# Kernel optimization log

Measured on AMD Instinct MI355X. Metric: run time of the kernel, lower is better.

The kernel has to match this reference:

```python
import jax, jax.numpy as jnp
import numpy as np

B, T, IN_DIM = 8, 1024, 512
NUM_HEADS, H_DIM = 8, 64
OUT_DIM = NUM_HEADS * H_DIM
MAX_POS = 512


def setup_inputs() -> dict:
    key = jax.random.key(0)
    ks = jax.random.split(key, 9)
    s = 0.02
    return {
        "x": jax.random.normal(ks[0], (B, T, IN_DIM), dtype=jnp.float32),
        "Wq": jax.random.normal(ks[1], (IN_DIM, OUT_DIM), dtype=jnp.float32) * s,
        "bq": jax.random.normal(ks[2], (OUT_DIM,), dtype=jnp.float32) * s,
        "Wkv": jax.random.normal(ks[3], (IN_DIM, 2 * OUT_DIM), dtype=jnp.float32) * s,
        "bkv": jax.random.normal(ks[4], (2 * OUT_DIM,), dtype=jnp.float32) * s,
        "Wout": jax.random.normal(ks[5], (OUT_DIM, IN_DIM), dtype=jnp.float32) * s,
        "bout": jax.random.normal(ks[6], (IN_DIM,), dtype=jnp.float32) * s,
        "rel_emb": jax.random.normal(ks[7], (2 * MAX_POS + 1, H_DIM), dtype=jnp.float32) * s,
    }


def reference(x, Wq, bq, Wkv, bkv, Wout, bout, rel_emb):
    b, t, _ = x.shape
    scale = H_DIM ** -0.5
    q = x @ Wq + bq                      # [b, t, H*D]
    kv = x @ Wkv + bkv                   # [b, t, 2*H*D]
    k, v = jnp.split(kv, 2, axis=-1)

    def split_heads(a):
        return a.reshape(b, t, NUM_HEADS, H_DIM).transpose(0, 2, 1, 3)  # b h t d

    q, k, v = map(split_heads, (q, k, v))
    dots = jnp.einsum("bhnd,bhmd->bhnm", q, k) * scale

    seq = jnp.arange(t)
    dist = jnp.clip(seq[:, None] - seq[None, :], -MAX_POS, MAX_POS) + MAX_POS  # [n, m]
    rel_pos = rel_emb[dist]              # [n, m, d]
    pos_attn = jnp.einsum("bhnd,nmd->bhnm", q, rel_pos) * scale

    attn = jax.nn.softmax(dots + pos_attn, axis=-1)
    out = jnp.einsum("bhnm,bhmd->bhnd", attn, v)
    out = out.transpose(0, 2, 1, 3).reshape(b, t, OUT_DIM)
    return out @ Wout + bout             # dropout p=0 -> identity
```

## Files before the change

kernel.cpp:

```cpp
#include <hip/hip_runtime.h>

#define BB 8
#define TT 1024
#define NH 8
#define HD 64
#define QT 128

typedef unsigned short u16;
typedef __attribute__((ext_vector_type(8))) short bf16x8;
typedef __attribute__((ext_vector_type(16))) float f32x16;

__device__ __forceinline__ float bf2f(u16 s) {
    union { unsigned u; float f; } v; v.u = ((unsigned)s) << 16; return v.f;
}
__device__ __forceinline__ u16 f2bf(float f) {
    union { float f; unsigned u; } v; v.f = f;
    unsigned r = (v.u + 0x7FFFu + ((v.u >> 16) & 1u)) >> 16;
    return (u16)r;
}
__device__ __forceinline__ float bperm(int byte_idx, float v) {
    union { float f; int i; } a; a.f = v;
    union { int i; float f; } b;
    b.i = __builtin_amdgcn_ds_bpermute(byte_idx, a.i);
    return b.f;
}
__device__ __forceinline__ void gload_lds16(const u16* g, u16* l) {
    __builtin_amdgcn_global_load_lds(
        (const __attribute__((address_space(1))) unsigned int*)g,
        (__attribute__((address_space(3))) unsigned int*)l, 16, 0, 0);
}

#define MFMA(a, b, c) __builtin_amdgcn_mfma_f32_32x32x16_bf16((a), (b), (c), 0, 0, 0)

#define NX4 1048576
#define NR4 16400
__global__ void cvt_misc(const float* __restrict__ x, const float* __restrict__ rel,
                         u16* __restrict__ xb, u16* __restrict__ relb)
{
    size_t i = (size_t)blockIdx.x * 256 + threadIdx.x;
    const float* src; u16* dst;
    if (i < NX4) { src = x; dst = xb; }
    else {
        i -= NX4;
        if (i >= NR4) return;
        src = rel; dst = relb;
    }
    float4 f = *(const float4*)(src + i * 4);
    ushort4 o;
    o.x = f2bf(f.x); o.y = f2bf(f.y); o.z = f2bf(f.z); o.w = f2bf(f.w);
    *(ushort4*)(dst + i * 4) = o;
}

__global__ __launch_bounds__(256) void cvt_wT(
    const float* __restrict__ Wq, const float* __restrict__ Wkv,
    const float* __restrict__ Wout,
    u16* __restrict__ WqT, u16* __restrict__ WkvT, u16* __restrict__ WoutT)
{
    __shared__ float tile[64][65];
    int bid = blockIdx.x;
    const float* W; u16* Wt; int N, kt, ct;
    if (bid < 64)       { W = Wq;   Wt = WqT;   N = 512;  kt = (bid >> 3) * 64; ct = (bid & 7) * 64; }
    else if (bid < 192) { bid -= 64;  W = Wkv;  Wt = WkvT; N = 1024; kt = (bid >> 4) * 64; ct = (bid & 15) * 64; }
    else                { bid -= 192; W = Wout; Wt = WoutT; N = 512;  kt = (bid >> 3) * 64; ct = (bid & 7) * 64; }

    const int tid = threadIdx.x;
#pragma unroll
    for (int i = 0; i < 16; i++) {
        int e = tid + i * 256;
        int r = e >> 6, c = e & 63;
        tile[r][c] = W[(size_t)(kt + r) * N + ct + c];
    }
    __syncthreads();
#pragma unroll
    for (int i = 0; i < 16; i++) {
        int e = tid + i * 256;
        int rr = e >> 6, cc = e & 63;
        Wt[(size_t)(ct + rr) * 512 + kt + cc] = f2bf(tile[cc][rr]);
    }
}

#define GEMM_STAGE(As, Bs, Abase, Bbase, k0)                                   \
    {                                                                          \
        const int wb16 = (tid & 192) * 8;   \
        _Pragma("unroll")                                                      \
        for (int i = 0; i < 4; i++) {                                          \
            int slot = i * 256 + tid;                                          \
            int row = slot >> 3;                                               \
            int c16 = (slot & 7) ^ (row & 7);                                  \
            gload_lds16(Abase + (size_t)row * 512 + (k0) + c16 * 8,            \
                        As + i * 2048 + wb16);                                 \
            gload_lds16(Bbase + (size_t)row * 512 + (k0) + c16 * 8,            \
                        Bs + i * 2048 + wb16);                                 \
        }                                                                      \
    }

#define GEMM_COMPUTE(As, Bs, ar_base, br_base)                                 \
    {                                                                          \
        _Pragma("unroll")                                                      \
        for (int ks = 0; ks < 4; ks++) {                                       \
            bf16x8 a0, a1, b0, b1;                                             \
            {                                                                  \
                int r0_ = (ar_base), r1_ = (ar_base) + 32;                     \
                int q0_ = (br_base), q1_ = (br_base) + 32;                     \
                a0 = *(const bf16x8*)(As + r0_ * 64 +                          \
                                      (((2 * ks + lh) ^ (r0_ & 7)) * 8));      \
                a1 = *(const bf16x8*)(As + r1_ * 64 +                          \
                                      (((2 * ks + lh) ^ (r1_ & 7)) * 8));      \
                b0 = *(const bf16x8*)(Bs + q0_ * 64 +                          \
                                      (((2 * ks + lh) ^ (q0_ & 7)) * 8));      \
                b1 = *(const bf16x8*)(Bs + q1_ * 64 +                          \
                                      (((2 * ks + lh) ^ (q1_ & 7)) * 8));      \
            }                                                                  \
            acc[0][0] = MFMA(a0, b0, acc[0][0]);                               \
            acc[0][1] = MFMA(a0, b1, acc[0][1]);                               \
            acc[1][0] = MFMA(a1, b0, acc[1][0]);                               \
            acc[1][1] = MFMA(a1, b1, acc[1][1]);                               \
        }                                                                      \
    }

__global__ __launch_bounds__(256) void gemm_qkv(
    const u16* __restrict__ A, const u16* __restrict__ Bt,
    const float* __restrict__ bq, const float* __restrict__ bkv,
    u16* __restrict__ oq, u16* __restrict__ ok, u16* __restrict__ ov)
{
    __shared__ __align__(16) u16 As[128 * 64];
    __shared__ __align__(16) u16 Bs[128 * 64];

    const int tid = threadIdx.x;
    const int lane = tid & 63, w = tid >> 6;
    const int l31 = lane & 31, lh = lane >> 5;
    const int wr = w & 1, wc = w >> 1;
    const int row0 = blockIdx.x * 128 + 64 * wr;
    const int c0g  = blockIdx.y * 128 + 64 * wc;

    const u16* Abase = A  + (size_t)blockIdx.x * 128 * 512;
    const u16* Bbase = Bt + (size_t)blockIdx.y * 128 * 512;
    const int ar_base = 64 * wr + l31;
    const int br_base = 64 * wc + l31;

    f32x16 acc[2][2];
#pragma unroll
    for (int i = 0; i < 2; i++)
#pragma unroll
        for (int j = 0; j < 2; j++)
#pragma unroll
            for (int e = 0; e < 16; e++) acc[i][j][e] = 0.f;

    for (int kk = 0; kk < 8; kk++) {
        GEMM_STAGE(As, Bs, Abase, Bbase, kk * 64);
        __syncthreads();
        GEMM_COMPUTE(As, Bs, ar_base, br_base);
        __syncthreads();
    }

    const int rbase = 4 * lh;
#pragma unroll
    for (int ri = 0; ri < 2; ri++) {
#pragma unroll
        for (int ci = 0; ci < 2; ci++) {
            const int r0 = row0 + 32 * ri;
            const int gc = c0g + 32 * ci + l31;
            if (gc < 512) {
                const float bv = bq[gc];
                const int h = gc >> 6, d = gc & 63;
#pragma unroll
                for (int rg = 0; rg < 16; rg++) {
                    int gr = r0 + (rg & 3) + 8 * (rg >> 2) + rbase;
                    int b = gr >> 10, t = gr & 1023;
                    oq[(((size_t)b * NH + h) * TT + t) * HD + d] =
                        f2bf((acc[ri][ci][rg] + bv) * 0.18033688f);
                }
            } else if (gc < 1024) {
                const float bv = bkv[gc - 512];
                const int h = (gc - 512) >> 6, d = gc & 63;
#pragma unroll
                for (int rg = 0; rg < 16; rg++) {
                    int gr = r0 + (rg & 3) + 8 * (rg >> 2) + rbase;
                    int b = gr >> 10, t = gr & 1023;
                    ok[(((size_t)b * NH + h) * TT + t) * HD + d] =
                        f2bf(acc[ri][ci][rg] + bv);
                }
            } else {
                const float bv = bkv[gc - 512];
                const int vcol = gc - 1024;
                const int h = vcol >> 6, d = vcol & 63;
                const int b = r0 >> 10;
                const int t0 = (r0 & 1023) + rbase;
                size_t base = (((size_t)b * NH + h) * HD + d) * TT;
#pragma unroll
                for (int g = 0; g < 4; g++) {
                    ushort4 p;
                    p.x = f2bf(acc[ri][ci][4 * g + 0] + bv);
                    p.y = f2bf(acc[ri][ci][4 * g + 1] + bv);
                    p.z = f2bf(acc[ri][ci][4 * g + 2] + bv);
                    p.w = f2bf(acc[ri][ci][4 * g + 3] + bv);
                    *(ushort4*)&ov[base + t0 + 8 * g] = p;
                }
            }
        }
    }
}

__global__ __launch_bounds__(256) void gemm_out(
    const u16* __restrict__ A, const u16* __restrict__ Bt,
    const float* __restrict__ bias, float* __restrict__ of)
{
    __shared__ __align__(16) u16 As[128 * 64];
    __shared__ __align__(16) u16 Bs[128 * 64];

    const int tid = threadIdx.x;
    const int lane = tid & 63, w = tid >> 6;
    const int l31 = lane & 31, lh = lane >> 5;
    const int wr = w & 1, wc = w >> 1;
    const int row0 = blockIdx.x * 128 + 64 * wr;
    const int c0g  = blockIdx.y * 128 + 64 * wc;

    const u16* Abase = A  + (size_t)blockIdx.x * 128 * 512;
    const u16* Bbase = Bt + (size_t)blockIdx.y * 128 * 512;
    const int ar_base = 64 * wr + l31;
    const int br_base = 64 * wc + l31;

    f32x16 acc[2][2];
#pragma unroll
    for (int i = 0; i < 2; i++)
#pragma unroll
        for (int j = 0; j < 2; j++)
#pragma unroll
            for (int e = 0; e < 16; e++) acc[i][j][e] = 0.f;

    for (int kk = 0; kk < 8; kk++) {
        GEMM_STAGE(As, Bs, Abase, Bbase, kk * 64);
        __syncthreads();
        GEMM_COMPUTE(As, Bs, ar_base, br_base);
        __syncthreads();
    }

    const int rbase = 4 * lh;
#pragma unroll
    for (int ri = 0; ri < 2; ri++) {
#pragma unroll
        for (int ci = 0; ci < 2; ci++) {
            const int gcol = c0g + 32 * ci + l31;
            const float bv = bias[gcol];
#pragma unroll
            for (int rg = 0; rg < 16; rg++) {
                int gr = row0 + 32 * ri + (rg & 3) + 8 * (rg >> 2) + rbase;
                of[(size_t)gr * 512 + gcol] = acc[ri][ci][rg] + bv;
            }
        }
    }
}

__global__ __launch_bounds__(256) void attn_mfma(
    const u16* __restrict__ q_ws, const u16* __restrict__ k_ws,
    const u16* __restrict__ v_ws, const u16* __restrict__ relb,
    u16* __restrict__ attn_out)
{
    __shared__ __align__(16) u16 GPs[4][32 * 104];

    const int tid  = threadIdx.x;
    const int lane = tid & 63;
    const int w    = tid >> 6;
    const int l31  = lane & 31;
    const int lh   = lane >> 5;
    const int bh   = blockIdx.x;
    const int n0   = blockIdx.y * QT;

    const unsigned lin = blockIdx.y * 64 + blockIdx.x;
    const int off = (int)((lin * 2654435761u) >> 24) & 15;

    bf16x8 a_q[4];
    {
        const u16* qp = q_ws + (((size_t)bh * TT) + n0 + 32 * w + l31) * HD + 8 * lh;
#pragma unroll
        for (int ks = 0; ks < 4; ks++)
            a_q[ks] = *(const bf16x8*)(qp + 16 * ks);
    }

    f32x16 O0, O1;
    float li[16];
#pragma unroll
    for (int i = 0; i < 16; i++) { O0[i] = 0.f; O1[i] = 0.f; li[i] = 0.f; }

    u16* Gw = GPs[w];
    const int rbase = 4 * lh;
    const u16* kbase = k_ws + (size_t)bh * TT * HD;
    const u16* vbase = v_ws + (size_t)bh * HD * TT;
    const int pbb = n0 + 449 + 32 * w;

    f32x16 zvec;
#pragma unroll
    for (int i = 0; i < 16; i++) zvec[i] = 0.f;
    int bidx16[16];
#pragma unroll
    for (int rg = 0; rg < 16; rg++) {
        int r = (rg & 3) + 8 * (rg >> 2) + rbase;
        bidx16[rg] = (((lh << 5) | ((r - l31 + 31) & 31))) << 2;
    }

    bf16x8 kf[8], rf[12];
    {
        const u16* kb = kbase + (size_t)(off * 64) * HD;
#pragma unroll
        for (int ks = 0; ks < 4; ks++) {
            const int doff = 16 * ks + 8 * lh;
            kf[2 * ks]     = *(const bf16x8*)(kb + (size_t)l31 * HD + doff);
            kf[2 * ks + 1] = *(const bf16x8*)(kb + (size_t)(l31 + 32) * HD + doff);
        }
    }
    f32x16 S0 = MFMA(a_q[0], kf[0], zvec);
    f32x16 S1 = MFMA(a_q[0], kf[1], zvec);
#pragma unroll
    for (int ks = 1; ks < 4; ks++) {
        S0 = MFMA(a_q[ks], kf[2 * ks], S0);
        S1 = MFMA(a_q[ks], kf[2 * ks + 1], S1);
    }
    {
        const int pb = pbb - off * 64;
#pragma unroll
        for (int gt = 0; gt < 3; gt++) {
            int p = pb + 32 * gt + l31;
            p = p < 0 ? 0 : (p > 1024 ? 1024 : p);
            const u16* rb = relb + (size_t)p * HD;
#pragma unroll
            for (int ks = 0; ks < 4; ks++)
                rf[4 * gt + ks] = *(const bf16x8*)(rb + 16 * ks + 8 * lh);
        }
    }
    {
        const u16* kb = kbase + (size_t)(((off + 1) & 15) * 64) * HD;
#pragma unroll
        for (int ks = 0; ks < 4; ks++) {
            const int doff = 16 * ks + 8 * lh;
            kf[2 * ks]     = *(const bf16x8*)(kb + (size_t)l31 * HD + doff);
            kf[2 * ks + 1] = *(const bf16x8*)(kb + (size_t)(l31 + 32) * HD + doff);
        }
    }

    for (int it = 0; it < 16; it++) {
        const int mt = (off + it) & 15;
        const int m0 = mt * 64;

        f32x16 gA = MFMA(a_q[0], rf[0], zvec);
        f32x16 gB = MFMA(a_q[0], rf[4], zvec);
        f32x16 gC = MFMA(a_q[0], rf[8], zvec);
#pragma unroll
        for (int ks = 1; ks < 4; ks++) {
            gA = MFMA(a_q[ks], rf[ks], gA);
            gB = MFMA(a_q[ks], rf[4 + ks], gB);
            gC = MFMA(a_q[ks], rf[8 + ks], gC);
        }

#pragma unroll
        for (int rg = 0; rg < 16; rg++) {
            int r = (rg & 3) + 8 * (rg >> 2) + rbase;
            float mS0 = (l31 >= r) ? gB[rg] : gC[rg];
            float mS1 = (l31 >= r) ? gA[rg] : gB[rg];
            S0[rg] += bperm(bidx16[rg], mS0);
            S1[rg] += bperm(bidx16[rg], mS1);
        }

        bf16x8 vf[8];
        {
            const u16* vb = vbase + m0;
#pragma unroll
            for (int ms = 0; ms < 4; ms++) {
                const int mg = 2 * ms + lh;
                vf[2 * ms]     = *(const bf16x8*)(vb + (size_t)l31 * TT + mg * 8);
                vf[2 * ms + 1] = *(const bf16x8*)(vb + (size_t)(l31 + 32) * TT + mg * 8);
            }
        }
        {
            const int m0n = ((off + it + 1) & 15) * 64;
            const int pb = pbb - m0n;
#pragma unroll
            for (int gt = 0; gt < 3; gt++) {
                int p = pb + 32 * gt + l31;
                p = p < 0 ? 0 : (p > 1024 ? 1024 : p);
                const u16* rb = relb + (size_t)p * HD;
#pragma unroll
                for (int ks = 0; ks < 4; ks++)
                    rf[4 * gt + ks] = *(const bf16x8*)(rb + 16 * ks + 8 * lh);
            }
        }

#pragma unroll
        for (int rg = 0; rg < 16; rg++) {
            float e0, e1;
            asm("v_exp_f32 %0, %1" : "=v"(e0) : "v"(S0[rg]));
            asm("v_exp_f32 %0, %1" : "=v"(e1) : "v"(S1[rg]));
            li[rg] += e0 + e1;
            unsigned pk;
            asm("v_cvt_pk_bf16_f32 %0, %1, %2" : "=v"(pk) : "v"(e0), "v"(e1));
            int r = (rg & 3) + 8 * (rg >> 2) + rbase;
            Gw[r * 104 + (((l31 >> 3) ^ (r & 7)) * 8) + (l31 & 7)] = (u16)pk;
            Gw[r * 104 + (((((l31 + 32) >> 3)) ^ (r & 7)) * 8) + (l31 & 7)] =
                (u16)(pk >> 16);
        }

        if (it < 15) {
            __builtin_amdgcn_s_setprio(1);
            S0 = MFMA(a_q[0], kf[0], zvec);
            S1 = MFMA(a_q[0], kf[1], zvec);
#pragma unroll
            for (int ks = 1; ks < 4; ks++) {
                S0 = MFMA(a_q[ks], kf[2 * ks], S0);
                S1 = MFMA(a_q[ks], kf[2 * ks + 1], S1);
            }
            __builtin_amdgcn_s_setprio(0);
            const int m0k = ((off + it + 2) & 15) * 64;
            const u16* kb = kbase + (size_t)m0k * HD;
#pragma unroll
            for (int ks = 0; ks < 4; ks++) {
                const int doff = 16 * ks + 8 * lh;
                kf[2 * ks]     = *(const bf16x8*)(kb + (size_t)l31 * HD + doff);
                kf[2 * ks + 1] = *(const bf16x8*)(kb + (size_t)(l31 + 32) * HD + doff);
            }
        }

        __builtin_amdgcn_s_setprio(1);
#pragma unroll
        for (int ms = 0; ms < 4; ms++) {
            const int mg = 2 * ms + lh;
            bf16x8 a_p = *(const bf16x8*)&Gw[l31 * 104 + ((mg ^ (l31 & 7)) * 8)];
            O0 = MFMA(a_p, vf[2 * ms], O0);
            O1 = MFMA(a_p, vf[2 * ms + 1], O1);
        }
        __builtin_amdgcn_s_setprio(0);
    }

#pragma unroll
    for (int rg = 0; rg < 16; rg++) {
        float rs = li[rg];
        rs += __shfl_xor(rs, 1);
        rs += __shfl_xor(rs, 2);
        rs += __shfl_xor(rs, 4);
        rs += __shfl_xor(rs, 8);
        rs += __shfl_xor(rs, 16);
        li[rg] = 1.0f / rs;
    }

    const int b = bh >> 3, h = bh & 7;
    u16* ob = attn_out + ((size_t)b * TT + n0 + 32 * w) * 512 + h * 64;
#pragma unroll
    for (int rg = 0; rg < 16; rg++) {
        int r = (rg & 3) + 8 * (rg >> 2) + rbase;
        ob[(size_t)r * 512 + l31]      = f2bf(O0[rg] * li[rg]);
        ob[(size_t)r * 512 + l31 + 32] = f2bf(O1[rg] * li[rg]);
    }
}

extern "C" void kernel_launch(void* const* d_in, const int* in_sizes, int n_in,
                              void* d_out, int out_size, void* d_ws, size_t ws_size,
                              hipStream_t stream)
{
    const float* x    = (const float*)d_in[0];
    const float* Wq   = (const float*)d_in[1];
    const float* bq   = (const float*)d_in[2];
    const float* Wkv  = (const float*)d_in[3];
    const float* bkv  = (const float*)d_in[4];
    const float* Wout = (const float*)d_in[5];
    const float* bout = (const float*)d_in[6];
    const float* rel  = (const float*)d_in[7];
    float* out = (float*)d_out;

    char* ws = (char*)d_ws;
    const size_t MB = 1024 * 1024;
    u16*   q_wsb  = (u16*)(ws);
    u16*   k_wsb  = (u16*)(ws + 8 * MB);
    u16*   v_wsb  = (u16*)(ws + 16 * MB);
    u16*   x_bf   = (u16*)(ws + 24 * MB);
    u16*   a_wsb  = (u16*)(ws + 32 * MB);
    u16*   relb   = (u16*)(ws + 40 * MB);
    u16*   WT_all = (u16*)(ws + 41 * MB);
    u16*   WoutT  = (u16*)(ws + 42 * MB + 512 * 1024);

    cvt_misc<<<(NX4 + NR4 + 255) / 256, 256, 0, stream>>>(x, rel, x_bf, relb);
    cvt_wT<<<256, 256, 0, stream>>>(Wq, Wkv, Wout, WT_all, WT_all + 512 * 512, WoutT);

    gemm_qkv<<<dim3(64, 12), 256, 0, stream>>>(
        x_bf, WT_all, bq, bkv, q_wsb, k_wsb, v_wsb);

    attn_mfma<<<dim3(64, 8), 256, 0, stream>>>(
        q_wsb, k_wsb, v_wsb, relb, a_wsb);

    gemm_out<<<dim3(64, 4), 256, 0, stream>>>(a_wsb, WoutT, bout, out);
}
```

Before: 222.4 us.

## Merge conversion kernels, narrow output GEMM tiles, reuse rel-pos fragments in attention

The two conversion kernels are merged into one launch to save a launch gap. The output GEMM tile shrinks from 128 to 64 columns, doubling the grid to 512 blocks for better CU occupancy at the cost of reloading A tiles more often. The attention kernel drops the hashed per-block starting offset and walks key tiles in order, so one of the three rel-pos fragment groups can be carried over from the previous iteration and only two are reloaded per tile. The in-order walk may cause more L2/channel contention, since all blocks now read the same K tiles at the same time.

```diff
diff --git a/kernel.cpp b/kernel.cpp
--- a/kernel.cpp
+++ b/kernel.cpp
@@ -34,36 +34,39 @@
 
 #define NX4 1048576
 #define NR4 16400
-__global__ void cvt_misc(const float* __restrict__ x, const float* __restrict__ rel,
-                         u16* __restrict__ xb, u16* __restrict__ relb)
-{
-    size_t i = (size_t)blockIdx.x * 256 + threadIdx.x;
-    const float* src; u16* dst;
-    if (i < NX4) { src = x; dst = xb; }
-    else {
-        i -= NX4;
-        if (i >= NR4) return;
-        src = rel; dst = relb;
-    }
-    float4 f = *(const float4*)(src + i * 4);
-    ushort4 o;
-    o.x = f2bf(f.x); o.y = f2bf(f.y); o.z = f2bf(f.z); o.w = f2bf(f.w);
-    *(ushort4*)(dst + i * 4) = o;
-}
-
-__global__ __launch_bounds__(256) void cvt_wT(
+#define CVT_MISC_BLOCKS 4161
+__global__ __launch_bounds__(256) void cvt_all(
+    const float* __restrict__ x, const float* __restrict__ rel,
     const float* __restrict__ Wq, const float* __restrict__ Wkv,
     const float* __restrict__ Wout,
+    u16* __restrict__ xb, u16* __restrict__ relb,
     u16* __restrict__ WqT, u16* __restrict__ WkvT, u16* __restrict__ WoutT)
 {
     __shared__ float tile[64][65];
-    int bid = blockIdx.x;
+    const int tid = threadIdx.x;
+
+    if (blockIdx.x < CVT_MISC_BLOCKS) {
+        size_t i = (size_t)blockIdx.x * 256 + tid;
+        const float* src; u16* dst;
+        if (i < NX4) { src = x; dst = xb; }
+        else {
+            i -= NX4;
+            if (i >= NR4) return;
+            src = rel; dst = relb;
+        }
+        float4 f = *(const float4*)(src + i * 4);
+        ushort4 o;
+        o.x = f2bf(f.x); o.y = f2bf(f.y); o.z = f2bf(f.z); o.w = f2bf(f.w);
+        *(ushort4*)(dst + i * 4) = o;
+        return;
+    }
+
+    int bid = blockIdx.x - CVT_MISC_BLOCKS;
     const float* W; u16* Wt; int N, kt, ct;
     if (bid < 64)       { W = Wq;   Wt = WqT;   N = 512;  kt = (bid >> 3) * 64; ct = (bid & 7) * 64; }
     else if (bid < 192) { bid -= 64;  W = Wkv;  Wt = WkvT; N = 1024; kt = (bid >> 4) * 64; ct = (bid & 15) * 64; }
     else                { bid -= 192; W = Wout; Wt = WoutT; N = 512;  kt = (bid >> 3) * 64; ct = (bid & 7) * 64; }
 
-    const int tid = threadIdx.x;
 #pragma unroll
     for (int i = 0; i < 16; i++) {
         int e = tid + i * 256;
@@ -206,48 +209,67 @@
     const float* __restrict__ bias, float* __restrict__ of)
 {
     __shared__ __align__(16) u16 As[128 * 64];
-    __shared__ __align__(16) u16 Bs[128 * 64];
+    __shared__ __align__(16) u16 Bs[64 * 64];
 
     const int tid = threadIdx.x;
     const int lane = tid & 63, w = tid >> 6;
     const int l31 = lane & 31, lh = lane >> 5;
     const int wr = w & 1, wc = w >> 1;
     const int row0 = blockIdx.x * 128 + 64 * wr;
-    const int c0g  = blockIdx.y * 128 + 64 * wc;
 
     const u16* Abase = A  + (size_t)blockIdx.x * 128 * 512;
-    const u16* Bbase = Bt + (size_t)blockIdx.y * 128 * 512;
+    const u16* Bbase = Bt + (size_t)blockIdx.y * 64 * 512;
     const int ar_base = 64 * wr + l31;
-    const int br_base = 64 * wc + l31;
-
-    f32x16 acc[2][2];
-#pragma unroll
-    for (int i = 0; i < 2; i++)
-#pragma unroll
-        for (int j = 0; j < 2; j++)
-#pragma unroll
-            for (int e = 0; e < 16; e++) acc[i][j][e] = 0.f;
+    const int br_base = 32 * wc + l31;
+
+    f32x16 acc0, acc1;
+#pragma unroll
+    for (int i = 0; i < 16; i++) { acc0[i] = 0.f; acc1[i] = 0.f; }
 
     for (int kk = 0; kk < 8; kk++) {
-        GEMM_STAGE(As, Bs, Abase, Bbase, kk * 64);
+        {
+            const int wb16 = (tid & 192) * 8;
+#pragma unroll
+            for (int i = 0; i < 4; i++) {
+                int slot = i * 256 + tid;
+                int row = slot >> 3;
+                int c16 = (slot & 7) ^ (row & 7);
+                gload_lds16(Abase + (size_t)row * 512 + kk * 64 + c16 * 8,
+                            As + i * 2048 + wb16);
+            }
+#pragma unroll
+            for (int i = 0; i < 2; i++) {
+                int slot = i * 256 + tid;
+                int row = slot >> 3;
+                int c16 = (slot & 7) ^ (row & 7);
+                gload_lds16(Bbase + (size_t)row * 512 + kk * 64 + c16 * 8,
+                            Bs + i * 2048 + wb16);
+            }
+        }
         __syncthreads();
-        GEMM_COMPUTE(As, Bs, ar_base, br_base);
+#pragma unroll
+        for (int ks = 0; ks < 4; ks++) {
+            int r0_ = ar_base, r1_ = ar_base + 32, q0_ = br_base;
+            bf16x8 a0 = *(const bf16x8*)(As + r0_ * 64 +
+                                         (((2 * ks + lh) ^ (r0_ & 7)) * 8));
+            bf16x8 a1 = *(const bf16x8*)(As + r1_ * 64 +
+                                         (((2 * ks + lh) ^ (r1_ & 7)) * 8));
+            bf16x8 b0 = *(const bf16x8*)(Bs + q0_ * 64 +
+                                         (((2 * ks + lh) ^ (q0_ & 7)) * 8));
+            acc0 = MFMA(a0, b0, acc0);
+            acc1 = MFMA(a1, b0, acc1);
+        }
         __syncthreads();
     }
 
     const int rbase = 4 * lh;
-#pragma unroll
-    for (int ri = 0; ri < 2; ri++) {
-#pragma unroll
-        for (int ci = 0; ci < 2; ci++) {
-            const int gcol = c0g + 32 * ci + l31;
-            const float bv = bias[gcol];
-#pragma unroll
-            for (int rg = 0; rg < 16; rg++) {
-                int gr = row0 + 32 * ri + (rg & 3) + 8 * (rg >> 2) + rbase;
-                of[(size_t)gr * 512 + gcol] = acc[ri][ci][rg] + bv;
-            }
-        }
+    const int gcol = blockIdx.y * 64 + 32 * wc + l31;
+    const float bv = bias[gcol];
+#pragma unroll
+    for (int rg = 0; rg < 16; rg++) {
+        int gr = row0 + (rg & 3) + 8 * (rg >> 2) + rbase;
+        of[(size_t)gr * 512 + gcol]        = acc0[rg] + bv;
+        of[(size_t)(gr + 32) * 512 + gcol] = acc1[rg] + bv;
     }
 }
 
@@ -266,9 +288,6 @@
     const int bh   = blockIdx.x;
     const int n0   = blockIdx.y * QT;
 
-    const unsigned lin = blockIdx.y * 64 + blockIdx.x;
-    const int off = (int)((lin * 2654435761u) >> 24) & 15;
-
     bf16x8 a_q[4];
     {
         const u16* qp = q_ws + (((size_t)bh * TT) + n0 + 32 * w + l31) * HD + 8 * lh;
@@ -299,8 +318,32 @@
     }
 
     bf16x8 kf[8], rf[12];
+#pragma unroll
+    for (int ks = 0; ks < 4; ks++) {
+        const int doff = 16 * ks + 8 * lh;
+        kf[2 * ks]     = *(const bf16x8*)(kbase + (size_t)l31 * HD + doff);
+        kf[2 * ks + 1] = *(const bf16x8*)(kbase + (size_t)(l31 + 32) * HD + doff);
+    }
+    f32x16 S0 = MFMA(a_q[0], kf[0], zvec);
+    f32x16 S1 = MFMA(a_q[0], kf[1], zvec);
+#pragma unroll
+    for (int ks = 1; ks < 4; ks++) {
+        S0 = MFMA(a_q[ks], kf[2 * ks], S0);
+        S1 = MFMA(a_q[ks], kf[2 * ks + 1], S1);
+    }
     {
-        const u16* kb = kbase + (size_t)(off * 64) * HD;
+#pragma unroll
+        for (int gt = 0; gt < 3; gt++) {
+            int p = pbb + 32 * gt + l31;
+            p = p < 0 ? 0 : (p > 1024 ? 1024 : p);
+            const u16* rb = relb + (size_t)p * HD;
+#pragma unroll
+            for (int ks = 0; ks < 4; ks++)
+                rf[4 * gt + ks] = *(const bf16x8*)(rb + 16 * ks + 8 * lh);
+        }
+    }
+    {
+        const u16* kb = kbase + (size_t)64 * HD;
 #pragma unroll
         for (int ks = 0; ks < 4; ks++) {
             const int doff = 16 * ks + 8 * lh;
@@ -308,37 +351,8 @@
             kf[2 * ks + 1] = *(const bf16x8*)(kb + (size_t)(l31 + 32) * HD + doff);
         }
     }
-    f32x16 S0 = MFMA(a_q[0], kf[0], zvec);
-    f32x16 S1 = MFMA(a_q[0], kf[1], zvec);
-#pragma unroll
-    for (int ks = 1; ks < 4; ks++) {
-        S0 = MFMA(a_q[ks], kf[2 * ks], S0);
-        S1 = MFMA(a_q[ks], kf[2 * ks + 1], S1);
-    }
-    {
-        const int pb = pbb - off * 64;
-#pragma unroll
-        for (int gt = 0; gt < 3; gt++) {
-            int p = pb + 32 * gt + l31;
-            p = p < 0 ? 0 : (p > 1024 ? 1024 : p);
-            const u16* rb = relb + (size_t)p * HD;
-#pragma unroll
-            for (int ks = 0; ks < 4; ks++)
-                rf[4 * gt + ks] = *(const bf16x8*)(rb + 16 * ks + 8 * lh);
-        }
-    }
-    {
-        const u16* kb = kbase + (size_t)(((off + 1) & 15) * 64) * HD;
-#pragma unroll
-        for (int ks = 0; ks < 4; ks++) {
-            const int doff = 16 * ks + 8 * lh;
-            kf[2 * ks]     = *(const bf16x8*)(kb + (size_t)l31 * HD + doff);
-            kf[2 * ks + 1] = *(const bf16x8*)(kb + (size_t)(l31 + 32) * HD + doff);
-        }
-    }
-
-    for (int it = 0; it < 16; it++) {
-        const int mt = (off + it) & 15;
+
+    for (int mt = 0; mt < 16; mt++) {
         const int m0 = mt * 64;
 
         f32x16 gA = MFMA(a_q[0], rf[0], zvec);
@@ -349,6 +363,24 @@
             gA = MFMA(a_q[ks], rf[ks], gA);
             gB = MFMA(a_q[ks], rf[4 + ks], gB);
             gC = MFMA(a_q[ks], rf[8 + ks], gC);
+        }
+
+        rf[8]  = rf[0];
+        rf[9]  = rf[1];
+        rf[10] = rf[2];
+        rf[11] = rf[3];
+        {
+            const int m0n = (mt < 15) ? m0 + 64 : 0;
+            const int pb = pbb - m0n;
+            int p0 = pb + l31;       p0 = p0 < 0 ? 0 : (p0 > 1024 ? 1024 : p0);
+            int p1 = pb + 32 + l31;  p1 = p1 < 0 ? 0 : (p1 > 1024 ? 1024 : p1);
+            const u16* rb0 = relb + (size_t)p0 * HD;
+            const u16* rb1 = relb + (size_t)p1 * HD;
+#pragma unroll
+            for (int ks = 0; ks < 4; ks++) {
+                rf[ks]     = *(const bf16x8*)(rb0 + 16 * ks + 8 * lh);
+                rf[4 + ks] = *(const bf16x8*)(rb1 + 16 * ks + 8 * lh);
+            }
         }
 
 #pragma unroll
@@ -368,19 +400,6 @@
                 const int mg = 2 * ms + lh;
                 vf[2 * ms]     = *(const bf16x8*)(vb + (size_t)l31 * TT + mg * 8);
                 vf[2 * ms + 1] = *(const bf16x8*)(vb + (size_t)(l31 + 32) * TT + mg * 8);
-            }
-        }
-        {
-            const int m0n = ((off + it + 1) & 15) * 64;
-            const int pb = pbb - m0n;
-#pragma unroll
-            for (int gt = 0; gt < 3; gt++) {
-                int p = pb + 32 * gt + l31;
-                p = p < 0 ? 0 : (p > 1024 ? 1024 : p);
-                const u16* rb = relb + (size_t)p * HD;
-#pragma unroll
-                for (int ks = 0; ks < 4; ks++)
-                    rf[4 * gt + ks] = *(const bf16x8*)(rb + 16 * ks + 8 * lh);
             }
         }
 
@@ -398,7 +417,7 @@
                 (u16)(pk >> 16);
         }
 
-        if (it < 15) {
+        if (mt < 15) {
             __builtin_amdgcn_s_setprio(1);
             S0 = MFMA(a_q[0], kf[0], zvec);
             S1 = MFMA(a_q[0], kf[1], zvec);
@@ -408,7 +427,7 @@
                 S1 = MFMA(a_q[ks], kf[2 * ks + 1], S1);
             }
             __builtin_amdgcn_s_setprio(0);
-            const int m0k = ((off + it + 2) & 15) * 64;
+            const int m0k = (mt < 14) ? m0 + 128 : 0;
             const u16* kb = kbase + (size_t)m0k * HD;
 #pragma unroll
             for (int ks = 0; ks < 4; ks++) {
@@ -475,8 +494,9 @@
     u16*   WT_all = (u16*)(ws + 41 * MB);
     u16*   WoutT  = (u16*)(ws + 42 * MB + 512 * 1024);
 
-    cvt_misc<<<(NX4 + NR4 + 255) / 256, 256, 0, stream>>>(x, rel, x_bf, relb);
-    cvt_wT<<<256, 256, 0, stream>>>(Wq, Wkv, Wout, WT_all, WT_all + 512 * 512, WoutT);
+    cvt_all<<<CVT_MISC_BLOCKS + 256, 256, 0, stream>>>(
+        x, rel, Wq, Wkv, Wout, x_bf, relb,
+        WT_all, WT_all + 512 * 512, WoutT);
 
     gemm_qkv<<<dim3(64, 12), 256, 0, stream>>>(
         x_bf, WT_all, bq, bkv, q_wsb, k_wsb, v_wsb);
@@ -484,5 +504,5 @@
     attn_mfma<<<dim3(64, 8), 256, 0, stream>>>(
         q_wsb, k_wsb, v_wsb, relb, a_wsb);
 
-    gemm_out<<<dim3(64, 4), 256, 0, stream>>>(a_wsb, WoutT, bout, out);
-}
+    gemm_out<<<dim3(64, 8), 256, 0, stream>>>(a_wsb, WoutT, bout, out);
+}
```

New measurement: 208.1 us. 1.07x faster.
